# Performance work log

Hardware: AMD Instinct MI355X
Metric: run time of the kernel (lower is better)

Reference implementation:

```python
import jax, jax.numpy as jnp
import numpy as np

B, S, D = 2, 2048, 2048
H, HKV, HD = 32, 8, 64
G = H // HKV  # num_key_value_groups


def setup_inputs() -> dict:
    key = jax.random.key(0)
    ks = jax.random.split(key, 9)
    sc = 0.02
    return {
        "x": jax.random.normal(ks[0], (B, S, D), jnp.float32),
        "wq": jax.random.normal(ks[1], (H * HD, D), jnp.float32) * sc,
        "bq": jax.random.normal(ks[2], (H * HD,), jnp.float32) * sc,
        "wk": jax.random.normal(ks[3], (HKV * HD, D), jnp.float32) * sc,
        "bk": jax.random.normal(ks[4], (HKV * HD,), jnp.float32) * sc,
        "wv": jax.random.normal(ks[5], (HKV * HD, D), jnp.float32) * sc,
        "bv": jax.random.normal(ks[6], (HKV * HD,), jnp.float32) * sc,
        "wo": jax.random.normal(ks[7], (D, H * HD), jnp.float32) * sc,
        "bo": jax.random.normal(ks[8], (D,), jnp.float32) * sc,
    }


def reference(x, wq, bq, wk, bk, wv, bv, wo, bo):
    b, s, _ = x.shape
    # fused-QKV-style projections (nn.Linear: x @ W.T + b)
    q = (jnp.einsum("bsd,ed->bse", x, wq) + bq).reshape(b, s, H, HD)
    k = (jnp.einsum("bsd,ed->bse", x, wk) + bk).reshape(b, s, HKV, HD)
    v = (jnp.einsum("bsd,ed->bse", x, wv) + bv).reshape(b, s, HKV, HD)
    # (B, Hkv, G, S, hd): grouped query heads share a KV head — same math as
    # repeat_kv (expand+flatten) without materializing the expanded KV tensor
    q = q.transpose(0, 2, 1, 3).reshape(b, HKV, G, s, HD)
    k = k.transpose(0, 2, 1, 3)  # (B, Hkv, S, hd)
    v = v.transpose(0, 2, 1, 3)
    scale = 1.0 / jnp.sqrt(jnp.asarray(HD, x.dtype))
    scores = jnp.einsum("bkgqd,bktd->bkgqt", q, k) * scale  # (B,Hkv,G,S,S)
    causal = jnp.tril(jnp.ones((s, s), bool))
    scores = jnp.where(causal, scores, jnp.asarray(-jnp.inf, scores.dtype))
    probs = jax.nn.softmax(scores, axis=-1)
    o = jnp.einsum("bkgqt,bktd->bkgqd", probs, v)  # (B,Hkv,G,S,hd)
    o = o.reshape(b, H, s, HD).transpose(0, 2, 1, 3).reshape(b, s, H * HD)
    return jnp.einsum("bse,de->bsd", o, wo) + bo
```

## Files before the change

kernel.cpp:

```cpp
#include <hip/hip_runtime.h>
#include <hip/hip_bf16.h>
#include <cmath>

#define B_   2
#define S_   2048
#define D_   2048
#define H_   32
#define HKV_ 8
#define HD_  64

using bf16 = __hip_bfloat16;
typedef __bf16    bf16x8 __attribute__((ext_vector_type(8)));
typedef float     floatx4 __attribute__((ext_vector_type(4)));
typedef _Float16  half4 __attribute__((ext_vector_type(4)));
typedef _Float16  half8 __attribute__((ext_vector_type(8)));
typedef _Float16  half2v __attribute__((ext_vector_type(2)));

#if __has_builtin(__builtin_amdgcn_exp2f)
#define EXP2(x) __builtin_amdgcn_exp2f(x)
#else
#define EXP2(x) exp2f(x)
#endif

#define QSCALE 0.18033688011112042f

__device__ inline void async16(const void* g, void* l) {
  __builtin_amdgcn_global_load_lds(
      (const __attribute__((address_space(1))) void*)g,
      (__attribute__((address_space(3))) void*)l, 16, 0, 0);
}

__device__ inline half2v pkrtz(float a, float b) {
  return __builtin_bit_cast(half2v, __builtin_amdgcn_cvt_pkrtz(a, b));
}

#define MFMA32B(a, b, c) __builtin_amdgcn_mfma_f32_16x16x32_bf16((a), (b), (c), 0, 0, 0)
#define MFMA16H(a, b, c) __builtin_amdgcn_mfma_f32_16x16x16f16((a), (b), (c), 0, 0, 0)

#define BARX() { asm volatile("" ::: "memory"); __builtin_amdgcn_s_barrier(); \
                 asm volatile("" ::: "memory"); }
#define LGKM0() asm volatile("s_waitcnt lgkmcnt(0)" ::: "memory")

__global__ void f2b_all(const float* __restrict__ x,  const float* __restrict__ wq,
                        const float* __restrict__ wk, const float* __restrict__ wv,
                        const float* __restrict__ wo,
                        bf16* __restrict__ xb,  bf16* __restrict__ wqb,
                        bf16* __restrict__ wkb, bf16* __restrict__ wvb,
                        bf16* __restrict__ wob) {
  const int i = blockIdx.x * blockDim.x + threadIdx.x;
  const float* src; bf16* dst; int off; float scale = 1.0f;
  if (i < 1048576)      { src = x;  dst = xb;  off = 0; }
  else if (i < 1572864) { src = wq; dst = wqb; off = 1048576; scale = QSCALE; }
  else if (i < 1703936) { src = wk; dst = wkb; off = 1572864; }
  else if (i < 1835008) { src = wv; dst = wvb; off = 1703936; }
  else                  { src = wo; dst = wob; off = 1835008; }
  const int j = i - off;
  float4 a  = ((const float4*)src)[2 * j];
  float4 b2 = ((const float4*)src)[2 * j + 1];
  alignas(16) bf16 t[8];
  t[0] = __float2bfloat16(a.x * scale);  t[1] = __float2bfloat16(a.y * scale);
  t[2] = __float2bfloat16(a.z * scale);  t[3] = __float2bfloat16(a.w * scale);
  t[4] = __float2bfloat16(b2.x * scale); t[5] = __float2bfloat16(b2.y * scale);
  t[6] = __float2bfloat16(b2.z * scale); t[7] = __float2bfloat16(b2.w * scale);
  ((uint4*)dst)[j] = *(const uint4*)t;
}

__global__ __launch_bounds__(512, 2)
void gemm_qkv8(const bf16* __restrict__ xb, const bf16* __restrict__ Wcat,
               const float* __restrict__ bq, const float* __restrict__ bk,
               const float* __restrict__ bv,
               bf16* __restrict__ Qo, bf16* __restrict__ Ko,
               _Float16* __restrict__ VG) {
  constexpr int NT = D_ / 64;
  __shared__ bf16 L[65536];

  const int id = blockIdx.x;
  const int bn = id & 7;
  const int bm = id >> 3;

  const int tid = threadIdx.x;
  const int wid = tid >> 6, lane = tid & 63;
  const int lm = lane & 15, quad = lane >> 4;
  const int wm = wid >> 2, wn = wid & 3;

  const int cOff = (quad * 8) ^ (((lm >> 3) & 1) << 4);
  const bf16* LA0 = L + (wm * 64 + lm) * 32 + cOff;
  const bf16* LB0 = L + 8192 + (wn * 96 + lm) * 32 + cOff;

  const int r0 = tid >> 2;
  const int csrc = ((tid & 3) * 8) ^ (((tid >> 5) & 1) << 4);
  const bf16* Asrc = xb   + (size_t)(bm * 128 + r0) * D_ + csrc;
  const bf16* Bs0  = Wcat + (size_t)(bn * 384 + r0) * D_ + csrc;
  const bf16* Bs1  = Bs0 + (size_t)128 * D_;
  const bf16* Bs2  = Bs0 + (size_t)256 * D_;
  bf16* Ld = L + tid * 8;

  floatx4 acc[4][6] = {};

#define STG_A(tt, hh, DB)  async16(Asrc + (tt) * 64 + (hh) * 32, (DB) + (hh) * 4096)
#define STG_B0(tt, hh, DB) async16(Bs0  + (tt) * 64 + (hh) * 32, (DB) + 8192 + (hh) * 12288)
#define STG_B1(tt, hh, DB) async16(Bs1  + (tt) * 64 + (hh) * 32, (DB) + 8192 + (hh) * 12288 + 4096)
#define STG_B2(tt, hh, DB) async16(Bs2  + (tt) * 64 + (hh) * 32, (DB) + 8192 + (hh) * 12288 + 8192)

  STG_A(0, 0, Ld); STG_B0(0, 0, Ld); STG_B1(0, 0, Ld); STG_B2(0, 0, Ld);
  STG_A(0, 1, Ld); STG_B0(0, 1, Ld); STG_B1(0, 1, Ld); STG_B2(0, 1, Ld);
  STG_A(1, 0, Ld + 32768); STG_B0(1, 0, Ld + 32768);
  STG_B1(1, 0, Ld + 32768); STG_B2(1, 0, Ld + 32768);
  asm volatile("s_waitcnt vmcnt(8)" ::: "memory");
  BARX();

  auto tile = [&](int t, const int BUF) __attribute__((always_inline)) {
    const bf16* LA = LA0 + BUF;
    const bf16* LB = LB0 + BUF;
    bf16* SD  = Ld + BUF;
    bf16* SDo = Ld + (BUF ^ 32768);
    const bool s1 = (t + 1) < NT, s2 = (t + 2) < NT;
    bf16x8 aF[4], bF[6];

#pragma unroll
    for (int i = 0; i < 4; ++i) aF[i] = *(const bf16x8*)(LA + i * 512);
#pragma unroll
    for (int i = 0; i < 6; ++i) bF[i] = *(const bf16x8*)(LB + i * 512);
    if (s1) { STG_A(t + 1, 1, SDo); STG_B0(t + 1, 1, SDo);
              STG_B1(t + 1, 1, SDo); STG_B2(t + 1, 1, SDo); }
    BARX(); LGKM0();
    __builtin_amdgcn_s_setprio(1);
#pragma unroll
    for (int mi = 0; mi < 4; ++mi)
#pragma unroll
      for (int ni = 0; ni < 6; ++ni)
        acc[mi][ni] = MFMA32B(bF[ni], aF[mi], acc[mi][ni]);
    __builtin_amdgcn_s_setprio(0);
    if (s1) { asm volatile("s_waitcnt vmcnt(8)" ::: "memory"); }
    else    { asm volatile("s_waitcnt vmcnt(0)" ::: "memory"); }
    BARX();

#pragma unroll
    for (int i = 0; i < 4; ++i) aF[i] = *(const bf16x8*)(LA + 4096 + i * 512);
#pragma unroll
    for (int i = 0; i < 6; ++i) bF[i] = *(const bf16x8*)(LB + 12288 + i * 512);
    if (s2) { STG_A(t + 2, 0, SD); STG_B0(t + 2, 0, SD);
              STG_B1(t + 2, 0, SD); STG_B2(t + 2, 0, SD); }
    BARX(); LGKM0();
    __builtin_amdgcn_s_setprio(1);
#pragma unroll
    for (int mi = 0; mi < 4; ++mi)
#pragma unroll
      for (int ni = 0; ni < 6; ++ni)
        acc[mi][ni] = MFMA32B(bF[ni], aF[mi], acc[mi][ni]);
    __builtin_amdgcn_s_setprio(0);
    if (s2)      { asm volatile("s_waitcnt vmcnt(8)" ::: "memory"); }
    else if (s1) { asm volatile("s_waitcnt vmcnt(4)" ::: "memory"); }
    else         { asm volatile("s_waitcnt vmcnt(0)" ::: "memory"); }
    BARX();
  };

  for (int t = 0; t < NT; t += 2) { tile(t, 0); tile(t + 1, 32768); }

#undef STG_A
#undef STG_B0
#undef STG_B1
#undef STG_B2

#pragma unroll
  for (int mi = 0; mi < 4; ++mi) {
    const int row = bm * 128 + wm * 64 + mi * 16 + lm;
#pragma unroll
    for (int ni = 0; ni < 6; ++ni) {
      const int colf = bn * 384 + wn * 96 + ni * 16;
      const int col0 = colf + quad * 4;
      if (colf < 2048) {
        float4 bv4 = *(const float4*)&bq[col0];
        alignas(8) bf16 t4[4];
#pragma unroll
        for (int r = 0; r < 4; ++r)
          t4[r] = __float2bfloat16(acc[mi][ni][r] + ((const float*)&bv4)[r] * QSCALE);
        *(uint2*)&Qo[(size_t)row * (H_ * HD_) + col0] = *(const uint2*)t4;
      } else if (colf < 2560) {
        const int ck = col0 - 2048;
        float4 bv4 = *(const float4*)&bk[ck];
        alignas(8) bf16 t4[4];
#pragma unroll
        for (int r = 0; r < 4; ++r)
          t4[r] = __float2bfloat16(acc[mi][ni][r] + ((const float*)&bv4)[r]);
        *(uint2*)&Ko[(size_t)row * (HKV_ * HD_) + ck] = *(const uint2*)t4;
      } else {
        const int cv = col0 - 2560;
        const int kvh = cv >> 6, hd = cv & 63;
        const int nh = hd >> 4;
        const int bb = row >> 11, s2 = row & 2047;
        const int tl = s2 >> 6, kvin = s2 & 63;
        const int kc = kvin >> 4, qd = (kvin >> 2) & 3, j = kvin & 3;
        const size_t base = ((size_t)((bb * 8 + kvh) * 32 + tl) << 12) +
                            (size_t)(((kc * 2 + (nh >> 1)) * 4 + qd) * 128 +
                                     (nh & 1) * 4 + j);
        float4 bv4 = *(const float4*)&bv[cv];
#pragma unroll
        for (int r = 0; r < 4; ++r)
          VG[base + (size_t)(quad * 4 + r) * 8] =
              (_Float16)(acc[mi][ni][r] + ((const float*)&bv4)[r]);
      }
    }
  }
}

__global__ __launch_bounds__(512, 2)
void gemm_o8(const bf16* __restrict__ A, const bf16* __restrict__ Bm,
             const float* __restrict__ bias, float* __restrict__ C) {
  constexpr int NT = D_ / 64;
  constexpr int BUFE = 24576;
  __shared__ bf16 L[2 * BUFE];

  const int id = blockIdx.x;
  const int bn = id & 7;
  const int bm = id >> 3;

  const int tid = threadIdx.x;
  const int wid = tid >> 6, lane = tid & 63;
  const int lm = lane & 15, quad = lane >> 4;
  const int wm = wid >> 2, wn = wid & 3;

  const int cOff = (quad * 8) ^ (((lm >> 3) & 1) << 4);
  const bf16* LA0 = L + (wm * 64 + lm) * 32 + cOff;
  const bf16* LB0 = L + 4096 + (wn * 64 + lm) * 32 + cOff;

  const int r0 = tid >> 2;
  const int csrc = ((tid & 3) * 8) ^ (((tid >> 5) & 1) << 4);
  const bf16* Asrc = A  + (size_t)(bm * 128 + r0) * D_ + csrc;
  const bf16* Bs0  = Bm + (size_t)(bn * 256 + r0) * D_ + csrc;
  const bf16* Bs1  = Bs0 + (size_t)128 * D_;
  bf16* Ld = L + tid * 8;

  floatx4 acc[4][4] = {};

#define STG_A(tt, hh, DB)  async16(Asrc + (tt) * 64 + (hh) * 32, (DB) + (hh) * 12288)
#define STG_B0(tt, hh, DB) async16(Bs0  + (tt) * 64 + (hh) * 32, (DB) + 4096 + (hh) * 12288)
#define STG_B1(tt, hh, DB) async16(Bs1  + (tt) * 64 + (hh) * 32, (DB) + 8192 + (hh) * 12288)

  STG_A(0, 0, Ld); STG_B0(0, 0, Ld); STG_B1(0, 0, Ld);
  STG_A(0, 1, Ld); STG_B0(0, 1, Ld); STG_B1(0, 1, Ld);
  STG_A(1, 0, Ld + BUFE); STG_B0(1, 0, Ld + BUFE); STG_B1(1, 0, Ld + BUFE);
  asm volatile("s_waitcnt vmcnt(6)" ::: "memory");
  BARX();

  auto tile = [&](int t, const int BUF) __attribute__((always_inline)) {
    const bf16* LA = LA0 + BUF;
    const bf16* LB = LB0 + BUF;
    bf16* SD  = Ld + BUF;
    bf16* SDo = Ld + (BUF ^ BUFE);
    const bool s1 = (t + 1) < NT, s2 = (t + 2) < NT;
    bf16x8 aF[4], bF[4];

#pragma unroll
    for (int i = 0; i < 4; ++i) aF[i] = *(const bf16x8*)(LA + i * 512);
#pragma unroll
    for (int i = 0; i < 4; ++i) bF[i] = *(const bf16x8*)(LB + i * 512);
    if (s1) { STG_A(t + 1, 1, SDo); STG_B0(t + 1, 1, SDo); STG_B1(t + 1, 1, SDo); }
    BARX(); LGKM0();
    __builtin_amdgcn_s_setprio(1);
#pragma unroll
    for (int mi = 0; mi < 4; ++mi)
#pragma unroll
      for (int ni = 0; ni < 4; ++ni)
        acc[mi][ni] = MFMA32B(bF[ni], aF[mi], acc[mi][ni]);
    __builtin_amdgcn_s_setprio(0);
    if (s1) { asm volatile("s_waitcnt vmcnt(6)" ::: "memory"); }
    else    { asm volatile("s_waitcnt vmcnt(0)" ::: "memory"); }
    BARX();

#pragma unroll
    for (int i = 0; i < 4; ++i) aF[i] = *(const bf16x8*)(LA + 12288 + i * 512);
#pragma unroll
    for (int i = 0; i < 4; ++i) bF[i] = *(const bf16x8*)(LB + 12288 + i * 512);
    if (s2) { STG_A(t + 2, 0, SD); STG_B0(t + 2, 0, SD); STG_B1(t + 2, 0, SD); }
    BARX(); LGKM0();
    __builtin_amdgcn_s_setprio(1);
#pragma unroll
    for (int mi = 0; mi < 4; ++mi)
#pragma unroll
      for (int ni = 0; ni < 4; ++ni)
        acc[mi][ni] = MFMA32B(bF[ni], aF[mi], acc[mi][ni]);
    __builtin_amdgcn_s_setprio(0);
    if (s2)      { asm volatile("s_waitcnt vmcnt(6)" ::: "memory"); }
    else if (s1) { asm volatile("s_waitcnt vmcnt(3)" ::: "memory"); }
    else         { asm volatile("s_waitcnt vmcnt(0)" ::: "memory"); }
    BARX();
  };

  for (int t = 0; t < NT; t += 2) { tile(t, 0); tile(t + 1, BUFE); }

#undef STG_A
#undef STG_B0
#undef STG_B1

#pragma unroll
  for (int mi = 0; mi < 4; ++mi) {
    const int row = bm * 128 + wm * 64 + mi * 16 + lm;
#pragma unroll
    for (int ni = 0; ni < 4; ++ni) {
      const int col0 = bn * 256 + wn * 64 + ni * 16 + quad * 4;
      float4 bv4 = *(const float4*)&bias[col0];
      float4 o4;
      o4.x = acc[mi][ni][0] + bv4.x; o4.y = acc[mi][ni][1] + bv4.y;
      o4.z = acc[mi][ni][2] + bv4.z; o4.w = acc[mi][ni][3] + bv4.w;
      *(float4*)&C[(size_t)row * D_ + col0] = o4;
    }
  }
}

__global__ __launch_bounds__(256, 5)
void attn_kernel(const bf16* __restrict__ Q, const bf16* __restrict__ K,
                 const _Float16* __restrict__ VG, bf16* __restrict__ O) {
  const int tid = threadIdx.x;
  const int wid = tid >> 6, lane = tid & 63;
  const int lm = lane & 15, quad = lane >> 4;

  const int n   = blockIdx.y * 64 + blockIdx.x;
  const int x3  = n & 7, b1 = (n >> 3) & 1;
  const int pair = n >> 4;
  const int grp  = x3 * 2 + b1;
  const int b    = grp >> 3, kvh = grp & 7;
  const int head = kvh * 4 + wid;

  const int hi = 127 - pair, lo = pair;
  const int nt_hi = (hi >> 2) + 1;
  const int nt_lo = (lo >> 2) + 1;

  __shared__ bf16     Ks[2 * 64 * 64];
  __shared__ _Float16 Vs[2 * 64 * 64];

  const int tb[2] = {hi * 16, lo * 16};

  bf16x8 qf[2][2];
#pragma unroll
  for (int tt = 0; tt < 2; ++tt) {
    const size_t qg = ((size_t)(b * S_ + tb[tt] + lm)) * (H_ * HD_) + head * HD_;
#pragma unroll
    for (int kf = 0; kf < 2; ++kf)
      qf[tt][kf] = *(const bf16x8*)&Q[qg + kf * 32 + quad * 8];
  }

  half4 onesh;
#pragma unroll
  for (int j = 0; j < 4; ++j) onesh[j] = (_Float16)1.0f;

  floatx4 o_acc[2][4] = {};
  floatx4 lacc[2] = {};

  auto stage = [&](int t, int buf) {
    const int tr = tid >> 2;
    const int tc = (tid & 3) * 8;
#pragma unroll
    for (int c = 0; c < 2; ++c) {
      async16(&K[(size_t)(b * S_ + t * 64 + tr) * (HKV_ * HD_) + kvh * HD_ + c * 32 + tc],
              &Ks[buf * 4096 + c * 2048 + tid * 8]);
      async16(&VG[((size_t)(grp * 32 + t) << 12) + c * 2048 + tid * 8],
              &Vs[buf * 4096 + c * 2048 + tid * 8]);
    }
  };

  stage(0, 0);

  for (int t = 0; t < nt_hi; ++t) {
    const int cur = t & 1;
    asm volatile("s_waitcnt vmcnt(0)" ::: "memory");
    __syncthreads();
    if (t + 1 < nt_hi) stage(t + 1, cur ^ 1);

    const bf16*     Kb = &Ks[cur * 4096];
    const _Float16* Vb = &Vs[cur * 4096];
    const int t0 = t * 64;
    const int nact = (t < nt_lo) ? 2 : 1;

    int kcmax[2], kcross[2];
#pragma unroll
    for (int tt = 0; tt < 2; ++tt) {
      const int rel = tb[tt] + 15 - t0;
      kcmax[tt]  = (tt < nact) ? ((rel >> 4) >= 3 ? 4 : (rel >> 4) + 1) : 0;
      kcross[tt] = rel >> 4;
    }

    half4 ps[2] = {};

#pragma unroll
    for (int kc = 0; kc < 4; ++kc) {
      if (kc >= kcmax[0]) break;
      bf16x8 kb0 = *(const bf16x8*)&Kb[(kc * 16 + lm) * 32 + quad * 8];
      bf16x8 kb1 = *(const bf16x8*)&Kb[2048 + (kc * 16 + lm) * 32 + quad * 8];

      floatx4 sT[2];
      __builtin_amdgcn_s_setprio(1);
#pragma unroll
      for (int tt = 0; tt < 2; ++tt) {
        if (kc >= kcmax[tt]) continue;
        floatx4 s0 = {};
        s0 = MFMA32B(kb0, qf[tt][0], s0);
        sT[tt] = MFMA32B(kb1, qf[tt][1], s0);
      }
      __builtin_amdgcn_s_setprio(0);

      half8 v0 = *(const half8*)&Vb[(kc * 8 + quad) * 128 + lm * 8];
      half8 v1 = *(const half8*)&Vb[(kc * 8 + 4 + quad) * 128 + lm * 8];
      half4 v0l = __builtin_shufflevector(v0, v0, 0, 1, 2, 3);
      half4 v0h = __builtin_shufflevector(v0, v0, 4, 5, 6, 7);
      half4 v1l = __builtin_shufflevector(v1, v1, 0, 1, 2, 3);
      half4 v1h = __builtin_shufflevector(v1, v1, 4, 5, 6, 7);

      half4 pbk[2];
#pragma unroll
      for (int tt = 0; tt < 2; ++tt) {
        if (kc >= kcmax[tt]) continue;
        floatx4 s = sT[tt];
        if (kc == kcross[tt]) {
          const int qrel = tb[tt] + lm - t0;
#pragma unroll
          for (int r = 0; r < 4; ++r)
            if (kc * 16 + quad * 4 + r > qrel) s[r] = -__builtin_inff();
        }
        half2v c0 = pkrtz(EXP2(s[0]), EXP2(s[1]));
        half2v c1 = pkrtz(EXP2(s[2]), EXP2(s[3]));
        half4 pk = __builtin_shufflevector(c0, c1, 0, 1, 2, 3);
        pbk[tt] = pk;
        ps[tt] += pk;
      }

      __builtin_amdgcn_s_setprio(1);
#pragma unroll
      for (int tt = 0; tt < 2; ++tt) {
        if (kc >= kcmax[tt]) continue;
        o_acc[tt][0] = MFMA16H(v0l, pbk[tt], o_acc[tt][0]);
        o_acc[tt][1] = MFMA16H(v0h, pbk[tt], o_acc[tt][1]);
        o_acc[tt][2] = MFMA16H(v1l, pbk[tt], o_acc[tt][2]);
        o_acc[tt][3] = MFMA16H(v1h, pbk[tt], o_acc[tt][3]);
      }
      __builtin_amdgcn_s_setprio(0);
    }

#pragma unroll
    for (int tt = 0; tt < 2; ++tt)
      if (kcmax[tt]) lacc[tt] = MFMA16H(onesh, ps[tt], lacc[tt]);
  }

#pragma unroll
  for (int tt = 0; tt < 2; ++tt) {
    const float rl = 1.f / lacc[tt][0];
    const size_t rowg = (size_t)(b * S_ + tb[tt] + lm);
#pragma unroll
    for (int nh = 0; nh < 4; ++nh) {
      alignas(8) bf16 tmp[4];
#pragma unroll
      for (int r = 0; r < 4; ++r)
        tmp[r] = __float2bfloat16(o_acc[tt][nh][r] * rl);
      *(uint2*)&O[rowg * (H_ * HD_) + head * HD_ + nh * 16 + quad * 4] = *(uint2*)tmp;
    }
  }
}

extern "C" void kernel_launch(void* const* d_in, const int* in_sizes, int n_in,
                              void* d_out, int out_size, void* d_ws, size_t ws_size,
                              hipStream_t stream) {
  (void)in_sizes; (void)n_in; (void)out_size; (void)ws_size;
  const float* x  = (const float*)d_in[0];
  const float* wq = (const float*)d_in[1];
  const float* bq = (const float*)d_in[2];
  const float* wk = (const float*)d_in[3];
  const float* bk = (const float*)d_in[4];
  const float* wv = (const float*)d_in[5];
  const float* bv = (const float*)d_in[6];
  const float* wo = (const float*)d_in[7];
  const float* bo = (const float*)d_in[8];
  float* out = (float*)d_out;

  const int M = B_ * S_;
  const int E = H_ * HD_;
  const int EKV = HKV_ * HD_;

  char* ws = (char*)d_ws;
  size_t off = 0;
  auto alloc = [&](size_t bytes) {
    char* p = ws + off;
    off += (bytes + 255) & ~(size_t)255;
    return p;
  };
  bf16* xb   = (bf16*)alloc((size_t)M * D_ * 2);
  bf16* Wcat = (bf16*)alloc((size_t)(E + 2 * EKV) * D_ * 2);
  bf16* wob  = (bf16*)alloc((size_t)D_ * E * 2);
  bf16* Qb   = (bf16*)alloc((size_t)M * E * 2);
  bf16* Kb   = (bf16*)alloc((size_t)M * EKV * 2);
  _Float16* VG = (_Float16*)alloc((size_t)M * EKV * 2);
  bf16* Ob   = (bf16*)alloc((size_t)M * E * 2);

  bf16* wqb = Wcat;
  bf16* wkb = Wcat + (size_t)E * D_;
  bf16* wvb = Wcat + (size_t)(E + EKV) * D_;

  f2b_all<<<9216, 256, 0, stream>>>(x, wq, wk, wv, wo, xb, wqb, wkb, wvb, wob);

  gemm_qkv8<<<dim3(256), dim3(512), 0, stream>>>(xb, Wcat, bq, bk, bv,
                                                 Qb, Kb, VG);

  attn_kernel<<<dim3(64, 16), 256, 0, stream>>>(Qb, Kb, VG, Ob);

  gemm_o8<<<dim3(256), dim3(512), 0, stream>>>(Ob, wob, bo, out);
}
```

Before: 284.9 us.

## Halve QKV GEMM tile width to 128x192 with 256 threads and swizzled block order

The QKV projection GEMM now uses 128x192 output tiles computed by 4 waves (256 threads) instead of 128x384 tiles on 8 waves. This doubles the grid to 512 blocks and shrinks the LDS footprint, which should fill all CUs and allow more blocks per CU. Block IDs are remapped so that neighbouring blocks share the same weight column tile, with the aim of improving L2 reuse. The staging macros and vmcnt wait counts are adjusted to match the new load pattern. In exchange, each block reuses its A tile across a narrower N range, which raises total global and L2 traffic for A.

```diff
diff --git a/kernel.cpp b/kernel.cpp
--- a/kernel.cpp
+++ b/kernel.cpp
@@ -65,23 +65,25 @@
   ((uint4*)dst)[j] = *(const uint4*)t;
 }
 
-__global__ __launch_bounds__(512, 2)
+__global__ __launch_bounds__(256, 2)
 void gemm_qkv8(const bf16* __restrict__ xb, const bf16* __restrict__ Wcat,
                const float* __restrict__ bq, const float* __restrict__ bk,
                const float* __restrict__ bv,
                bf16* __restrict__ Qo, bf16* __restrict__ Ko,
                _Float16* __restrict__ VG) {
   constexpr int NT = D_ / 64;
-  __shared__ bf16 L[65536];
-
-  const int id = blockIdx.x;
-  const int bn = id & 7;
-  const int bm = id >> 3;
+  constexpr int BUFE = 20480;
+  __shared__ bf16 L[2 * BUFE];
+
+  const int id  = blockIdx.x;
+  const int swz = (id & 7) * 64 + (id >> 3);
+  const int bn  = swz >> 5;
+  const int bm  = swz & 31;
 
   const int tid = threadIdx.x;
   const int wid = tid >> 6, lane = tid & 63;
   const int lm = lane & 15, quad = lane >> 4;
-  const int wm = wid >> 2, wn = wid & 3;
+  const int wm = wid >> 1, wn = wid & 1;
 
   const int cOff = (quad * 8) ^ (((lm >> 3) & 1) << 4);
   const bf16* LA0 = L + (wm * 64 + lm) * 32 + cOff;
@@ -90,30 +92,30 @@
   const int r0 = tid >> 2;
   const int csrc = ((tid & 3) * 8) ^ (((tid >> 5) & 1) << 4);
   const bf16* Asrc = xb   + (size_t)(bm * 128 + r0) * D_ + csrc;
-  const bf16* Bs0  = Wcat + (size_t)(bn * 384 + r0) * D_ + csrc;
-  const bf16* Bs1  = Bs0 + (size_t)128 * D_;
-  const bf16* Bs2  = Bs0 + (size_t)256 * D_;
+  const bf16* Bsrc = Wcat + (size_t)(bn * 192 + r0) * D_ + csrc;
   bf16* Ld = L + tid * 8;
 
   floatx4 acc[4][6] = {};
 
-#define STG_A(tt, hh, DB)  async16(Asrc + (tt) * 64 + (hh) * 32, (DB) + (hh) * 4096)
-#define STG_B0(tt, hh, DB) async16(Bs0  + (tt) * 64 + (hh) * 32, (DB) + 8192 + (hh) * 12288)
-#define STG_B1(tt, hh, DB) async16(Bs1  + (tt) * 64 + (hh) * 32, (DB) + 8192 + (hh) * 12288 + 4096)
-#define STG_B2(tt, hh, DB) async16(Bs2  + (tt) * 64 + (hh) * 32, (DB) + 8192 + (hh) * 12288 + 8192)
-
-  STG_A(0, 0, Ld); STG_B0(0, 0, Ld); STG_B1(0, 0, Ld); STG_B2(0, 0, Ld);
-  STG_A(0, 1, Ld); STG_B0(0, 1, Ld); STG_B1(0, 1, Ld); STG_B2(0, 1, Ld);
-  STG_A(1, 0, Ld + 32768); STG_B0(1, 0, Ld + 32768);
-  STG_B1(1, 0, Ld + 32768); STG_B2(1, 0, Ld + 32768);
-  asm volatile("s_waitcnt vmcnt(8)" ::: "memory");
+#define STG_A(tt, hh, DB) { \
+    async16(Asrc + (tt) * 64 + (hh) * 32,                  (DB) + (hh) * 4096); \
+    async16(Asrc + (size_t)64 * D_ + (tt) * 64 + (hh) * 32, (DB) + (hh) * 4096 + 2048); }
+#define STG_B(tt, hh, DB) { \
+    async16(Bsrc + (tt) * 64 + (hh) * 32,                    (DB) + 8192 + (hh) * 6144); \
+    async16(Bsrc + (size_t)64 * D_ + (tt) * 64 + (hh) * 32,  (DB) + 8192 + (hh) * 6144 + 2048); \
+    async16(Bsrc + (size_t)128 * D_ + (tt) * 64 + (hh) * 32, (DB) + 8192 + (hh) * 6144 + 4096); }
+
+  STG_A(0, 0, Ld); STG_B(0, 0, Ld);
+  STG_A(0, 1, Ld); STG_B(0, 1, Ld);
+  STG_A(1, 0, Ld + BUFE); STG_B(1, 0, Ld + BUFE);
+  asm volatile("s_waitcnt vmcnt(10)" ::: "memory");
   BARX();
 
   auto tile = [&](int t, const int BUF) __attribute__((always_inline)) {
     const bf16* LA = LA0 + BUF;
     const bf16* LB = LB0 + BUF;
     bf16* SD  = Ld + BUF;
-    bf16* SDo = Ld + (BUF ^ 32768);
+    bf16* SDo = Ld + (BUF ^ BUFE);
     const bool s1 = (t + 1) < NT, s2 = (t + 2) < NT;
     bf16x8 aF[4], bF[6];
 
@@ -121,8 +123,7 @@
     for (int i = 0; i < 4; ++i) aF[i] = *(const bf16x8*)(LA + i * 512);
 #pragma unroll
     for (int i = 0; i < 6; ++i) bF[i] = *(const bf16x8*)(LB + i * 512);
-    if (s1) { STG_A(t + 1, 1, SDo); STG_B0(t + 1, 1, SDo);
-              STG_B1(t + 1, 1, SDo); STG_B2(t + 1, 1, SDo); }
+    if (s1) { STG_A(t + 1, 1, SDo); STG_B(t + 1, 1, SDo); }
     BARX(); LGKM0();
     __builtin_amdgcn_s_setprio(1);
 #pragma unroll
@@ -131,16 +132,15 @@
       for (int ni = 0; ni < 6; ++ni)
         acc[mi][ni] = MFMA32B(bF[ni], aF[mi], acc[mi][ni]);
     __builtin_amdgcn_s_setprio(0);
-    if (s1) { asm volatile("s_waitcnt vmcnt(8)" ::: "memory"); }
+    if (s1) { asm volatile("s_waitcnt vmcnt(10)" ::: "memory"); }
     else    { asm volatile("s_waitcnt vmcnt(0)" ::: "memory"); }
     BARX();
 
 #pragma unroll
     for (int i = 0; i < 4; ++i) aF[i] = *(const bf16x8*)(LA + 4096 + i * 512);
 #pragma unroll
-    for (int i = 0; i < 6; ++i) bF[i] = *(const bf16x8*)(LB + 12288 + i * 512);
-    if (s2) { STG_A(t + 2, 0, SD); STG_B0(t + 2, 0, SD);
-              STG_B1(t + 2, 0, SD); STG_B2(t + 2, 0, SD); }
+    for (int i = 0; i < 6; ++i) bF[i] = *(const bf16x8*)(LB + 6144 + i * 512);
+    if (s2) { STG_A(t + 2, 0, SD); STG_B(t + 2, 0, SD); }
     BARX(); LGKM0();
     __builtin_amdgcn_s_setprio(1);
 #pragma unroll
@@ -149,25 +149,23 @@
       for (int ni = 0; ni < 6; ++ni)
         acc[mi][ni] = MFMA32B(bF[ni], aF[mi], acc[mi][ni]);
     __builtin_amdgcn_s_setprio(0);
-    if (s2)      { asm volatile("s_waitcnt vmcnt(8)" ::: "memory"); }
-    else if (s1) { asm volatile("s_waitcnt vmcnt(4)" ::: "memory"); }
+    if (s2)      { asm volatile("s_waitcnt vmcnt(10)" ::: "memory"); }
+    else if (s1) { asm volatile("s_waitcnt vmcnt(5)" ::: "memory"); }
     else         { asm volatile("s_waitcnt vmcnt(0)" ::: "memory"); }
     BARX();
   };
 
-  for (int t = 0; t < NT; t += 2) { tile(t, 0); tile(t + 1, 32768); }
+  for (int t = 0; t < NT; t += 2) { tile(t, 0); tile(t + 1, BUFE); }
 
 #undef STG_A
-#undef STG_B0
-#undef STG_B1
-#undef STG_B2
+#undef STG_B
 
 #pragma unroll
   for (int mi = 0; mi < 4; ++mi) {
     const int row = bm * 128 + wm * 64 + mi * 16 + lm;
 #pragma unroll
     for (int ni = 0; ni < 6; ++ni) {
-      const int colf = bn * 384 + wn * 96 + ni * 16;
+      const int colf = bn * 192 + wn * 96 + ni * 16;
       const int col0 = colf + quad * 4;
       if (colf < 2048) {
         float4 bv4 = *(const float4*)&bq[col0];
@@ -496,7 +494,7 @@
 
   f2b_all<<<9216, 256, 0, stream>>>(x, wq, wk, wv, wo, xb, wqb, wkb, wvb, wob);
 
-  gemm_qkv8<<<dim3(256), dim3(512), 0, stream>>>(xb, Wcat, bq, bk, bv,
+  gemm_qkv8<<<dim3(512), dim3(256), 0, stream>>>(xb, Wcat, bq, bk, bv,
                                                  Qb, Kb, VG);
 
   attn_kernel<<<dim3(64, 16), 256, 0, stream>>>(Qb, Kb, VG, Ob);
```

After: 288.8 us. Within noise of the previous version (+1.4%).
